# Optimization experiments

Measured on AMD Instinct MI355X. Metric: run time of the kernel, lower is better.

## Reference

```python
import jax, jax.numpy as jnp
import numpy as np


def _spectral_normalize(W):
    # spectral_norm divides the weight by its largest singular value
    sigma = jnp.linalg.norm(W, ord=2)
    return W / sigma


def setup_inputs() -> dict:
    key = jax.random.key(0)
    ks = jax.random.split(key, 8)
    B, C, H, W = 2, 64, 96, 96
    C8 = C // 8
    x = jax.random.normal(ks[0], (B, C, H, W), dtype=jnp.float32)
    Wq = jax.random.normal(ks[1], (C8, C), dtype=jnp.float32) * 0.1
    bq = jax.random.normal(ks[2], (C8,), dtype=jnp.float32) * 0.1
    Wk = jax.random.normal(ks[3], (C8, C), dtype=jnp.float32) * 0.1
    bk = jax.random.normal(ks[4], (C8,), dtype=jnp.float32) * 0.1
    Wv = jax.random.normal(ks[5], (C, C), dtype=jnp.float32) * 0.1
    bv = jax.random.normal(ks[6], (C,), dtype=jnp.float32) * 0.1
    gamma = jnp.ones((1,), dtype=jnp.float32)
    return {"x": x, "Wq": Wq, "bq": bq, "Wk": Wk, "bk": bk,
            "Wv": Wv, "bv": bv, "gamma": gamma}


def reference(x, Wq, bq, Wk, bk, Wv, bv, gamma):
    B, C, H, W = x.shape
    xf = x.reshape(B, C, H * W)                       # [B, C, N]
    Wq_n = _spectral_normalize(Wq)
    Wk_n = _spectral_normalize(Wk)
    Wv_n = _spectral_normalize(Wv)
    # 1x1 Conv1d == matmul over channel dim
    f = jnp.einsum('oc,bcn->bon', Wq_n, xf) + bq[None, :, None]   # [B, C/8, N]
    g = jnp.einsum('oc,bcn->bon', Wk_n, xf) + bk[None, :, None]   # [B, C/8, N]
    h = jnp.einsum('oc,bcn->bon', Wv_n, xf) + bv[None, :, None]   # [B, C, N]
    # scores[b,i,j] = sum_c f[b,c,i] * g[b,c,j];  softmax over dim=1 (i)
    scores = jnp.einsum('bci,bcj->bij', f, g)                      # [B, N, N]
    beta = jax.nn.softmax(scores, axis=1)
    # o[b,c,j] = sum_i h[b,c,i] * beta[b,i,j]
    o = gamma[0] * jnp.einsum('bci,bij->bcj', h, beta) + xf
    return o.reshape(B, C, H, W)
```

## Files before the change

kernel.cpp:

```cpp
#include <hip/hip_runtime.h>


#define N_PIX 9216
#define N_B   2
#define N_C   64

typedef _Float16 half8  __attribute__((ext_vector_type(8)));
typedef float    float4v __attribute__((ext_vector_type(4)));
typedef float    float16v __attribute__((ext_vector_type(16)));
typedef int      int4v  __attribute__((ext_vector_type(4)));

#define LOG2E 1.44269504088896340736f
#define EXP_SHIFT 12.0f

__global__ __launch_bounds__(64) void k_sigma(const float* __restrict__ Wq,
                                              const float* __restrict__ Wk,
                                              const float* __restrict__ Wv,
                                              float* __restrict__ sig,
                                              unsigned* __restrict__ maxKu) {
  __shared__ float G8[8][8];
  __shared__ float Wl[64 * 64];
  __shared__ _Float16 Wh[64 * 80];
  __shared__ _Float16 Gh[64 * 80];
  const int t = threadIdx.x;
  const int mat = blockIdx.x;
  if (mat == 0 && t < 2) maxKu[t] = 0u;
  if (mat < 2) {
    const float* W = (mat == 0) ? Wq : Wk;
    const int i = t >> 3, j = t & 7;
    float g = 0.f;
    for (int c = 0; c < 64; ++c) g += W[i * 64 + c] * W[j * 64 + c];
    G8[i][j] = g;
    __syncthreads();
    const int L = t & 7;
    float G0[8], Gr[8];
    for (int k = 0; k < 8; ++k) { G0[k] = G8[L][k]; Gr[k] = G0[k]; }
    for (int it = 0; it < 8; ++it) {
      float g2[8] = {0, 0, 0, 0, 0, 0, 0, 0};
      for (int k = 0; k < 8; ++k) {
        float gik = Gr[k];
        for (int jj = 0; jj < 8; ++jj) g2[jj] += gik * __shfl(Gr[jj], k, 64);
      }
      float mx = 0.f;
      for (int jj = 0; jj < 8; ++jj) mx = fmaxf(mx, fabsf(g2[jj]));
      for (int d = 1; d < 8; d <<= 1) mx = fmaxf(mx, __shfl_xor(mx, d, 64));
      float r = 1.f / mx;
      for (int jj = 0; jj < 8; ++jj) Gr[jj] = g2[jj] * r;
    }
    float u = 0.f;
    for (int jj = 0; jj < 8; ++jj) u += Gr[jj];
    float y = 0.f;
    for (int k = 0; k < 8; ++k) y += G0[k] * __shfl(u, k, 64);
    float nu = u * y, de = u * u;
    for (int d = 1; d < 8; d <<= 1) { nu += __shfl_xor(nu, d, 64); de += __shfl_xor(de, d, 64); }
    if (t == 0) sig[mat] = sqrtf(nu / de);
  } else {
    for (int idx = t; idx < 4096; idx += 64) Wl[idx] = Wv[idx];
    __syncthreads();
    for (int idx = t; idx < 4096; idx += 64) Wh[(idx >> 6) * 80 + (idx & 63)] = (_Float16)Wl[idx];
    __syncthreads();
    const int lane15 = t & 15, quad = t >> 4;
    half8 fr[4][2];
    for (int rb = 0; rb < 4; ++rb)
      for (int kc = 0; kc < 2; ++kc)
        fr[rb][kc] = *(const half8*)&Wh[(lane15 + 16 * rb) * 80 + 32 * kc + 8 * quad];
    float4v D[4][4];
    for (int mb = 0; mb < 4; ++mb) for (int nb = 0; nb < 4; ++nb) D[mb][nb] = (float4v){0.f, 0.f, 0.f, 0.f};
    for (int kc = 0; kc < 2; ++kc)
      for (int mb = 0; mb < 4; ++mb)
        for (int nb = 0; nb < 4; ++nb)
          D[mb][nb] = __builtin_amdgcn_mfma_f32_16x16x32_f16(fr[mb][kc], fr[nb][kc], D[mb][nb], 0, 0, 0);
    for (int it = 0; it < 8; ++it) {
      float mx = 0.f;
      for (int mb = 0; mb < 4; ++mb) for (int nb = 0; nb < 4; ++nb) for (int r = 0; r < 4; ++r)
        mx = fmaxf(mx, fabsf(D[mb][nb][r]));
      for (int d = 1; d < 64; d <<= 1) mx = fmaxf(mx, __shfl_xor(mx, d, 64));
      float rs = 1.f / mx;
      for (int mb = 0; mb < 4; ++mb) for (int nb = 0; nb < 4; ++nb) for (int r = 0; r < 4; ++r)
        Gh[(4 * quad + r + 16 * mb) * 80 + lane15 + 16 * nb] = (_Float16)(D[mb][nb][r] * rs);
      __syncthreads();
      if (it == 7) break;
      for (int rb = 0; rb < 4; ++rb)
        for (int kc = 0; kc < 2; ++kc)
          fr[rb][kc] = *(const half8*)&Gh[(lane15 + 16 * rb) * 80 + 32 * kc + 8 * quad];
      for (int mb = 0; mb < 4; ++mb) for (int nb = 0; nb < 4; ++nb) D[mb][nb] = (float4v){0.f, 0.f, 0.f, 0.f};
      for (int kc = 0; kc < 2; ++kc)
        for (int mb = 0; mb < 4; ++mb)
          for (int nb = 0; nb < 4; ++nb)
            D[mb][nb] = __builtin_amdgcn_mfma_f32_16x16x32_f16(fr[mb][kc], fr[nb][kc], D[mb][nb], 0, 0, 0);
      __syncthreads();
    }
    float u = 0.f;
    for (int c = 0; c < 64; ++c) u += (float)Gh[t * 80 + c];
    float z = 0.f;
    for (int i2 = 0; i2 < 64; ++i2) z += Wl[i2 * 64 + t] * __shfl(u, i2, 64);
    float nu = z * z, de = u * u;
    for (int d = 1; d < 64; d <<= 1) { nu += __shfl_xor(nu, d, 64); de += __shfl_xor(de, d, 64); }
    if (t == 0) sig[2] = sqrtf(nu / de);
  }
}

__global__ __launch_bounds__(256) void k_fgh(const float* __restrict__ x,
                                             const float* __restrict__ Wq, const float* __restrict__ bq,
                                             const float* __restrict__ Wk, const float* __restrict__ bk,
                                             const float* __restrict__ Wv, const float* __restrict__ bv,
                                             const float* __restrict__ sig,
                                             _Float16* __restrict__ K16,
                                             _Float16* __restrict__ Q16,
                                             _Float16* __restrict__ VT16,
                                             unsigned* __restrict__ maxKu) {
  __shared__ _Float16 Wsh[80 * 64];
  __shared__ float bsh[80];
  const int t = threadIdx.x;
  const float iq = LOG2E / sig[0], ik = 1.0f / sig[1], iv = 1.0f / sig[2];
  for (int idx = t; idx < 80 * 64; idx += 256) {
    const int m = idx >> 6, c = idx & 63;
    float v;
    if (m < 8)       v = Wq[m * 64 + c] * iq;
    else if (m < 16) v = Wk[(m - 8) * 64 + c] * ik;
    else             v = Wv[(m - 16) * 64 + c] * iv;
    Wsh[idx] = (_Float16)v;
  }
  if (t < 80) {
    float v;
    if (t < 8)       v = bq[t] * LOG2E;
    else if (t < 16) v = bk[t - 8];
    else             v = bv[t - 16];
    bsh[t] = v;
  }
  __syncthreads();
  const int wave = t >> 6;
  const int lane = t & 63;
  const int lane15 = lane & 15, quad = lane >> 4;
  const int tile = blockIdx.x * 4 + wave;
  const int b = tile / 576;
  const int n = (tile % 576) * 16 + lane15;
  half8 wf[5][2];
  for (int mb = 0; mb < 5; ++mb)
    for (int kc = 0; kc < 2; ++kc)
      wf[mb][kc] = *(const half8*)&Wsh[(lane15 + 16 * mb) * 64 + 32 * kc + 8 * quad];
  float4v acc[5];
  for (int mb = 0; mb < 5; ++mb) acc[mb] = *(const float4v*)&bsh[16 * mb + 4 * quad];
  const float* xb = x + (size_t)b * N_C * N_PIX;
  for (int kc = 0; kc < 2; ++kc) {
    half8 bf;
    for (int j = 0; j < 8; ++j)
      bf[j] = (_Float16)xb[(size_t)(32 * kc + 8 * quad + j) * N_PIX + n];
    for (int mb = 0; mb < 5; ++mb)
      acc[mb] = __builtin_amdgcn_mfma_f32_16x16x32_f16(wf[mb][kc], bf, acc[mb], 0, 0, 0);
  }
  {
    _Float16* dstK = K16 + ((size_t)b * N_PIX + n) * 8;
    _Float16* dstQ = Q16 + ((size_t)b * N_PIX + n) * 8;
    for (int r = 0; r < 4; ++r) {
      const int m = 4 * quad + r;
      const _Float16 v = (_Float16)acc[0][r];
      if (m < 8) dstK[m] = v; else dstQ[m - 8] = v;
    }
  }
  for (int mb = 1; mb < 5; ++mb)
    for (int r = 0; r < 4; ++r) {
      const int c = 4 * quad + r + 16 * (mb - 1);
      VT16[((size_t)b * N_C + c) * N_PIX + n] = (_Float16)acc[mb][r];
    }
  float sq = 0.f;
  if (quad < 2)
    for (int r = 0; r < 4; ++r) sq += acc[0][r] * acc[0][r];
  sq += __shfl_xor(sq, 16, 64);
  for (int d = 1; d < 64; d <<= 1) sq = fmaxf(sq, __shfl_xor(sq, d, 64));
  if (lane == 0) atomicMax(&maxKu[b], __float_as_uint(sq));
}


__device__ __forceinline__ void gload16(const _Float16* g, _Float16* l) {
  __builtin_amdgcn_global_load_lds(
      (const __attribute__((address_space(1))) void*)g,
      (__attribute__((address_space(3))) void*)l, 16, 0, 0);
}
#define VMWAIT5() asm volatile("s_waitcnt vmcnt(5)" ::: "memory")

__global__ __launch_bounds__(256, 4) void k_attn(const _Float16* __restrict__ K16,
                                                 const _Float16* __restrict__ Q16,
                                                 const _Float16* __restrict__ VT16,
                                                 const unsigned* __restrict__ maxKu,
                                                 float* __restrict__ Opart,
                                                 float* __restrict__ Lpart) {
  __shared__ __align__(16) _Float16 SM[4][5120];
  const int wave = threadIdx.x >> 6;
  const int lane = threadIdx.x & 63;
  const int q31 = lane & 31, hi = lane >> 5;
  const int tile = blockIdx.x;
  const int b = tile / 576;
  const int rm = tile % 576;
  const int jb = (rm >> 1) * 32;
  const int h = rm & 1;
  const int kh = h * (N_PIX / 2);
  const _Float16* Kb = K16 + (size_t)b * N_PIX * 8;
  const _Float16* Vb = VT16 + (size_t)b * N_C * N_PIX;
  _Float16* Rg = SM[wave];
  const int cl = lane >> 2, kk = lane & 3;
  const int gsw = (kk ^ ((cl >> 1) & 3)) * 8;
  const int vx = (q31 >> 1) & 3;
  const int voff00 = q31 * 32 + ((hi ^ vx) << 3);
  const int voff01 = q31 * 32 + (((2 + hi) ^ vx) << 3);
  const int voff10 = 1024 + voff00;
  const int voff11 = 1024 + voff01;

  half8 qf = {};
  if (hi == 0) qf = *(const half8*)(Q16 + ((size_t)b * N_PIX + jb + q31) * 8);
  const float maxK = sqrtf(__uint_as_float(maxKu[b]));
  float nq = 0.f;
#pragma unroll
  for (int j = 0; j < 8; ++j) nq += (float)qf[j] * (float)qf[j];
  nq += __shfl_xor(nq, 32, 64);
  const float M = sqrtf(nq) * maxK - EXP_SHIFT;
  float16v sinit;
#pragma unroll
  for (int r2 = 0; r2 < 16; ++r2) sinit[r2] = -M;

  float16v acc0 = {}, acc1 = {};
  float ls = 0.f;

#define STAGE(SLOT, I0)                                                          \
  {                                                                              \
    const int _i = (I0);                                                         \
    gload16(Kb + (size_t)(_i + q31) * 8, Rg + 4096 + (SLOT) * 512);              \
    gload16(Vb + (size_t)cl * N_PIX + _i + gsw,        Rg + (SLOT) * 2048);      \
    gload16(Vb + (size_t)(16 + cl) * N_PIX + _i + gsw, Rg + (SLOT) * 2048 + 512);\
    gload16(Vb + (size_t)(32 + cl) * N_PIX + _i + gsw, Rg + (SLOT) * 2048 + 1024);\
    gload16(Vb + (size_t)(48 + cl) * N_PIX + _i + gsw, Rg + (SLOT) * 2048 + 1536);\
  }

  STAGE(0, kh + 32 * wave)

#pragma unroll 1
  for (int r = 0; r < 36; ++r) {
    const int slot = r & 1, nslot = slot ^ 1;
    const int i1 = kh + ((r < 35) ? (128 * (r + 1) + 32 * wave) : (128 * 35 + 32 * wave));
    STAGE(nslot, i1)
    VMWAIT5();
    half8 kf = *(const half8*)&Rg[4096 + slot * 512 + q31 * 8];
    if (hi) kf = (half8){};
    float16v s = __builtin_amdgcn_mfma_f32_32x32x16_f16(kf, qf, sinit, 0, 0, 0);
    int pk[8];
#pragma unroll
    for (int u = 0; u < 8; ++u) {
      const float p0 = __builtin_amdgcn_exp2f(s[2 * u]);
      const float p1 = __builtin_amdgcn_exp2f(s[2 * u + 1]);
      ls += p0 + p1;
      pk[u] = __builtin_bit_cast(int, __builtin_amdgcn_cvt_pkrtz(p0, p1));
    }
    const int t0 = hi ? pk[0] : pk[2];
    const int t1 = hi ? pk[1] : pk[3];
    const int t2 = hi ? pk[4] : pk[6];
    const int t3 = hi ? pk[5] : pk[7];
    const int x0 = __shfl_xor(t0, 32, 64);
    const int x1 = __shfl_xor(t1, 32, 64);
    const int x2 = __shfl_xor(t2, 32, 64);
    const int x3 = __shfl_xor(t3, 32, 64);
    int4v B0i, B1i;
    B0i[0] = hi ? x0 : pk[0];  B0i[1] = hi ? x1 : pk[1];
    B0i[2] = hi ? pk[2] : x0;  B0i[3] = hi ? pk[3] : x1;
    B1i[0] = hi ? x2 : pk[4];  B1i[1] = hi ? x3 : pk[5];
    B1i[2] = hi ? pk[6] : x2;  B1i[3] = hi ? pk[7] : x3;
    const half8 P0 = __builtin_bit_cast(half8, B0i);
    const half8 P1 = __builtin_bit_cast(half8, B1i);
    const _Float16* Vs = Rg + slot * 2048;
    const half8 v00 = *(const half8*)&Vs[voff00];
    const half8 v01 = *(const half8*)&Vs[voff01];
    const half8 v10 = *(const half8*)&Vs[voff10];
    const half8 v11 = *(const half8*)&Vs[voff11];
    acc0 = __builtin_amdgcn_mfma_f32_32x32x16_f16(v00, P0, acc0, 0, 0, 0);
    acc0 = __builtin_amdgcn_mfma_f32_32x32x16_f16(v01, P1, acc0, 0, 0, 0);
    acc1 = __builtin_amdgcn_mfma_f32_32x32x16_f16(v10, P0, acc1, 0, 0, 0);
    acc1 = __builtin_amdgcn_mfma_f32_32x32x16_f16(v11, P1, acc1, 0, 0, 0);
  }
#undef STAGE
  asm volatile("s_waitcnt vmcnt(0)" ::: "memory");

  float* Ow = (float*)Rg;
  float* Lw = (float*)Rg + 1100;
  ls += __shfl_xor(ls, 32, 64);
  if (hi == 0) Lw[q31] = ls;
#pragma unroll
  for (int r2 = 0; r2 < 16; ++r2) Ow[lane * 17 + r2] = acc0[r2];
  __syncthreads();
  float ltot = 0.f;
#pragma unroll
  for (int w = 0; w < 4; ++w) ltot += ((const float*)SM[w])[1100 + q31];
  float* Op = Opart + (size_t)tile * 2048;
  if (wave == 0 && hi == 0) Lpart[tile * 32 + q31] = ltot;
#pragma unroll
  for (int r2 = 0; r2 < 16; ++r2) {
    float osum = 0.f;
#pragma unroll
    for (int w = 0; w < 4; ++w) osum += ((const float*)SM[w])[lane * 17 + r2];
    const int c = (r2 & 3) + 8 * (r2 >> 2) + 4 * hi;
    Op[c * 32 + q31] = osum;
  }
  __syncthreads();
#pragma unroll
  for (int r2 = 0; r2 < 16; ++r2) Ow[lane * 17 + r2] = acc1[r2];
  __syncthreads();
#pragma unroll
  for (int r2 = 0; r2 < 16; ++r2) {
    float osum = 0.f;
#pragma unroll
    for (int w = 0; w < 4; ++w) osum += ((const float*)SM[w])[lane * 17 + r2];
    const int c = 32 + (r2 & 3) + 8 * (r2 >> 2) + 4 * hi;
    Op[c * 32 + q31] = osum;
  }
}

__global__ __launch_bounds__(256) void k_merge(const float* __restrict__ Opart,
                                               const float* __restrict__ Lpart,
                                               const float* __restrict__ x,
                                               const float* __restrict__ gamma,
                                               float* __restrict__ out) {
  __shared__ float Ls[32];
  const int t2 = blockIdx.x;
  const int b = t2 / 288, jt = t2 % 288;
  const int jb = jt * 32;
  const int tile0 = b * 576 + jt * 2;
  const float gm = gamma[0];
  const int t = threadIdx.x;
  if (t < 32) Ls[t] = Lpart[tile0 * 32 + t] + Lpart[(tile0 + 1) * 32 + t];
  __syncthreads();
  const float* O0 = Opart + (size_t)tile0 * 2048;
  const float* O1 = O0 + 2048;
  const float* xb = x + (size_t)b * N_C * N_PIX;
  float* ob = out + (size_t)b * N_C * N_PIX;
#pragma unroll
  for (int k = 0; k < 8; ++k) {
    const int idx = t + 256 * k;
    const int c = idx >> 5, q = idx & 31;
    const size_t gi = (size_t)c * N_PIX + jb + q;
    ob[gi] = gm * (O0[idx] + O1[idx]) / Ls[q] + xb[gi];
  }
}

extern "C" void kernel_launch(void* const* d_in, const int* in_sizes, int n_in,
                              void* d_out, int out_size, void* d_ws, size_t ws_size,
                              hipStream_t stream) {
  const float* x     = (const float*)d_in[0];
  const float* Wq    = (const float*)d_in[1];
  const float* bq    = (const float*)d_in[2];
  const float* Wk    = (const float*)d_in[3];
  const float* bk    = (const float*)d_in[4];
  const float* Wv    = (const float*)d_in[5];
  const float* bv    = (const float*)d_in[6];
  const float* gamma = (const float*)d_in[7];
  float* out = (float*)d_out;

  char* ws = (char*)d_ws;
  float*    sig   = (float*)ws;
  unsigned* maxKu = (unsigned*)(ws + 16);
  _Float16* K16   = (_Float16*)(ws + 10752);
  _Float16* Q16   = (_Float16*)(ws + 10752 + 294912);
  _Float16* VT16  = (_Float16*)(ws + 10752 + 2 * 294912);
  float*    Opart = (float*)(ws + 2960384);
  float*    Lpart = (float*)(ws + 2960384 + 9437184);

  hipLaunchKernelGGL(k_sigma, dim3(3), dim3(64), 0, stream, Wq, Wk, Wv, sig, maxKu);
  hipLaunchKernelGGL(k_fgh, dim3(288), dim3(256), 0, stream,
                     x, Wq, bq, Wk, bk, Wv, bv, sig, K16, Q16, VT16, maxKu);
  hipLaunchKernelGGL(k_attn, dim3(1152), dim3(256), 0, stream, K16, Q16, VT16, maxKu, Opart, Lpart);
  hipLaunchKernelGGL(k_merge, dim3(576), dim3(256), 0, stream, Opart, Lpart, x, gamma, out);
}
```

Before: 171.9 us.

## Software-pipeline attention loop so PV MFMAs overlap next tile's exp

Restructures the attention main loop into a two-stage software pipeline. The PV MFMAs for the previous tile now run alongside the QK MFMA and exp/pack of the current tile, using ping-pong register sets and a manual unroll by two. All five LDS reads per step are issued together through inline asm with one lgkmcnt wait, and a drain step after the loop handles the last tile. This hides the exp and shuffle latency behind matrix work, at the cost of more live VGPRs, which may hurt occupancy under launch_bounds(256,4), and of inline asm that limits compiler scheduling.

```diff
diff --git a/kernel.cpp b/kernel.cpp
--- a/kernel.cpp
+++ b/kernel.cpp
@@ -178,6 +178,16 @@
       (__attribute__((address_space(3))) void*)l, 16, 0, 0);
 }
 #define VMWAIT5() asm volatile("s_waitcnt vmcnt(5)" ::: "memory")
+typedef const __attribute__((address_space(3))) _Float16* lds_cp;
+#define DS5(K, V0, V1, V2, V3, PK, PV0, PV1, PV2, PV3)                   \
+  asm volatile("ds_read_b128 %0, %5\n\t"                                 \
+               "ds_read_b128 %1, %6\n\t"                                 \
+               "ds_read_b128 %2, %7\n\t"                                 \
+               "ds_read_b128 %3, %8\n\t"                                 \
+               "ds_read_b128 %4, %9\n\t"                                 \
+               "s_waitcnt lgkmcnt(0)"                                    \
+               : "=&v"(K), "=&v"(V0), "=&v"(V1), "=&v"(V2), "=&v"(V3)    \
+               : "v"(PK), "v"(PV0), "v"(PV1), "v"(PV2), "v"(PV3) : "memory")
 
 __global__ __launch_bounds__(256, 4) void k_attn(const _Float16* __restrict__ K16,
                                                  const _Float16* __restrict__ Q16,
@@ -231,52 +241,76 @@
     gload16(Vb + (size_t)(48 + cl) * N_PIX + _i + gsw, Rg + (SLOT) * 2048 + 1536);\
   }
 
+  int4v Pa0 = {}, Pa1 = {}, Va0 = {}, Va1 = {}, Va2 = {}, Va3 = {};
+  int4v Pb0, Pb1, Vb0, Vb1, Vb2, Vb3;
+
+#define BODY(R, SLOT, NSLOT, PP0, PP1, VP0, VP1, VP2, VP3, PC0, PC1, VC0, VC1, VC2, VC3) \
+  {                                                                                      \
+    const int i1 = kh + (((R) < 35) ? (128 * ((R) + 1) + 32 * wave)                      \
+                                    : (128 * 35 + 32 * wave));                           \
+    STAGE(NSLOT, i1)                                                                     \
+    VMWAIT5();                                                                           \
+    int4v kfi;                                                                           \
+    {                                                                                    \
+      lds_cp pk  = (lds_cp)(Rg + 4096 + (SLOT) * 512 + q31 * 8);                         \
+      lds_cp pv0 = (lds_cp)(Rg + (SLOT) * 2048 + voff00);                                \
+      lds_cp pv1 = (lds_cp)(Rg + (SLOT) * 2048 + voff01);                                \
+      lds_cp pv2 = (lds_cp)(Rg + (SLOT) * 2048 + voff10);                                \
+      lds_cp pv3 = (lds_cp)(Rg + (SLOT) * 2048 + voff11);                                \
+      DS5(kfi, VC0, VC1, VC2, VC3, pk, pv0, pv1, pv2, pv3);                              \
+    }                                                                                    \
+    half8 kf = __builtin_bit_cast(half8, kfi);                                           \
+    if (hi) kf = (half8){};                                                              \
+    float16v s = __builtin_amdgcn_mfma_f32_32x32x16_f16(kf, qf, sinit, 0, 0, 0);         \
+                                        \
+    acc0 = __builtin_amdgcn_mfma_f32_32x32x16_f16(__builtin_bit_cast(half8, VP0),        \
+                                                  __builtin_bit_cast(half8, PP0), acc0, 0, 0, 0); \
+    acc0 = __builtin_amdgcn_mfma_f32_32x32x16_f16(__builtin_bit_cast(half8, VP1),        \
+                                                  __builtin_bit_cast(half8, PP1), acc0, 0, 0, 0); \
+    acc1 = __builtin_amdgcn_mfma_f32_32x32x16_f16(__builtin_bit_cast(half8, VP2),        \
+                                                  __builtin_bit_cast(half8, PP0), acc1, 0, 0, 0); \
+    acc1 = __builtin_amdgcn_mfma_f32_32x32x16_f16(__builtin_bit_cast(half8, VP3),        \
+                                                  __builtin_bit_cast(half8, PP1), acc1, 0, 0, 0); \
+                               \
+    int pkv[8];                                                                          \
+    _Pragma("unroll") for (int u = 0; u < 8; ++u) {                                      \
+      const float p0 = __builtin_amdgcn_exp2f(s[2 * u]);                                 \
+      const float p1 = __builtin_amdgcn_exp2f(s[2 * u + 1]);                             \
+      ls += p0 + p1;                                                                     \
+      pkv[u] = __builtin_bit_cast(int, __builtin_amdgcn_cvt_pkrtz(p0, p1));              \
+    }                                                                                    \
+    const int t0 = hi ? pkv[0] : pkv[2];                                                 \
+    const int t1 = hi ? pkv[1] : pkv[3];                                                 \
+    const int t2 = hi ? pkv[4] : pkv[6];                                                 \
+    const int t3 = hi ? pkv[5] : pkv[7];                                                 \
+    const int x0 = __shfl_xor(t0, 32, 64);                                               \
+    const int x1 = __shfl_xor(t1, 32, 64);                                               \
+    const int x2 = __shfl_xor(t2, 32, 64);                                               \
+    const int x3 = __shfl_xor(t3, 32, 64);                                               \
+    PC0[0] = hi ? x0 : pkv[0];  PC0[1] = hi ? x1 : pkv[1];                               \
+    PC0[2] = hi ? pkv[2] : x0;  PC0[3] = hi ? pkv[3] : x1;                               \
+    PC1[0] = hi ? x2 : pkv[4];  PC1[1] = hi ? x3 : pkv[5];                               \
+    PC1[2] = hi ? pkv[6] : x2;  PC1[3] = hi ? pkv[7] : x3;                               \
+  }
+
   STAGE(0, kh + 32 * wave)
-
 #pragma unroll 1
-  for (int r = 0; r < 36; ++r) {
-    const int slot = r & 1, nslot = slot ^ 1;
-    const int i1 = kh + ((r < 35) ? (128 * (r + 1) + 32 * wave) : (128 * 35 + 32 * wave));
-    STAGE(nslot, i1)
-    VMWAIT5();
-    half8 kf = *(const half8*)&Rg[4096 + slot * 512 + q31 * 8];
-    if (hi) kf = (half8){};
-    float16v s = __builtin_amdgcn_mfma_f32_32x32x16_f16(kf, qf, sinit, 0, 0, 0);
-    int pk[8];
-#pragma unroll
-    for (int u = 0; u < 8; ++u) {
-      const float p0 = __builtin_amdgcn_exp2f(s[2 * u]);
-      const float p1 = __builtin_amdgcn_exp2f(s[2 * u + 1]);
-      ls += p0 + p1;
-      pk[u] = __builtin_bit_cast(int, __builtin_amdgcn_cvt_pkrtz(p0, p1));
-    }
-    const int t0 = hi ? pk[0] : pk[2];
-    const int t1 = hi ? pk[1] : pk[3];
-    const int t2 = hi ? pk[4] : pk[6];
-    const int t3 = hi ? pk[5] : pk[7];
-    const int x0 = __shfl_xor(t0, 32, 64);
-    const int x1 = __shfl_xor(t1, 32, 64);
-    const int x2 = __shfl_xor(t2, 32, 64);
-    const int x3 = __shfl_xor(t3, 32, 64);
-    int4v B0i, B1i;
-    B0i[0] = hi ? x0 : pk[0];  B0i[1] = hi ? x1 : pk[1];
-    B0i[2] = hi ? pk[2] : x0;  B0i[3] = hi ? pk[3] : x1;
-    B1i[0] = hi ? x2 : pk[4];  B1i[1] = hi ? x3 : pk[5];
-    B1i[2] = hi ? pk[6] : x2;  B1i[3] = hi ? pk[7] : x3;
-    const half8 P0 = __builtin_bit_cast(half8, B0i);
-    const half8 P1 = __builtin_bit_cast(half8, B1i);
-    const _Float16* Vs = Rg + slot * 2048;
-    const half8 v00 = *(const half8*)&Vs[voff00];
-    const half8 v01 = *(const half8*)&Vs[voff01];
-    const half8 v10 = *(const half8*)&Vs[voff10];
-    const half8 v11 = *(const half8*)&Vs[voff11];
-    acc0 = __builtin_amdgcn_mfma_f32_32x32x16_f16(v00, P0, acc0, 0, 0, 0);
-    acc0 = __builtin_amdgcn_mfma_f32_32x32x16_f16(v01, P1, acc0, 0, 0, 0);
-    acc1 = __builtin_amdgcn_mfma_f32_32x32x16_f16(v10, P0, acc1, 0, 0, 0);
-    acc1 = __builtin_amdgcn_mfma_f32_32x32x16_f16(v11, P1, acc1, 0, 0, 0);
-  }
+  for (int j2 = 0; j2 < 18; ++j2) {
+    const int r = 2 * j2;
+    BODY(r,     0, 1, Pa0, Pa1, Va0, Va1, Va2, Va3, Pb0, Pb1, Vb0, Vb1, Vb2, Vb3)
+    BODY(r + 1, 1, 0, Pb0, Pb1, Vb0, Vb1, Vb2, Vb3, Pa0, Pa1, Va0, Va1, Va2, Va3)
+  }
+#undef BODY
 #undef STAGE
   asm volatile("s_waitcnt vmcnt(0)" ::: "memory");
+  acc0 = __builtin_amdgcn_mfma_f32_32x32x16_f16(__builtin_bit_cast(half8, Va0),
+                                                __builtin_bit_cast(half8, Pa0), acc0, 0, 0, 0);
+  acc0 = __builtin_amdgcn_mfma_f32_32x32x16_f16(__builtin_bit_cast(half8, Va1),
+                                                __builtin_bit_cast(half8, Pa1), acc0, 0, 0, 0);
+  acc1 = __builtin_amdgcn_mfma_f32_32x32x16_f16(__builtin_bit_cast(half8, Va2),
+                                                __builtin_bit_cast(half8, Pa0), acc1, 0, 0, 0);
+  acc1 = __builtin_amdgcn_mfma_f32_32x32x16_f16(__builtin_bit_cast(half8, Va3),
+                                                __builtin_bit_cast(half8, Pa1), acc1, 0, 0, 0);
 
   float* Ow = (float*)Rg;
   float* Lw = (float*)Rg + 1100;
```

Result: slower. 180.0 us (+4.7%).
